# Performance work log

Hardware: AMD Instinct MI355X
Metric: run time of the kernel (lower is better)

Reference implementation:

```python
import jax, jax.numpy as jnp
import numpy as np

DIM = 1024
HEADS = 16
DIM_HEAD = 64
INNER = HEADS * DIM_HEAD  # 1024
EPS = 1e-5


def setup_inputs() -> dict:
    key = jax.random.key(0)
    ks = jax.random.split(key, 5)
    x = jax.random.normal(ks[0], (4, 2048, DIM), dtype=jnp.float32)
    ln_gamma = jnp.ones((DIM,), dtype=jnp.float32)
    ln_beta = jnp.zeros((DIM,), dtype=jnp.float32)
    # nn.Linear weights ~ U(-1/sqrt(fan_in), 1/sqrt(fan_in)); stored as (out, in) in torch,
    # here kept as (in, out) for x @ W.
    lim = 1.0 / np.sqrt(DIM)
    w_qkv = jax.random.uniform(ks[1], (DIM, 3 * INNER), minval=-lim, maxval=lim, dtype=jnp.float32)
    lim2 = 1.0 / np.sqrt(INNER)
    w_out = jax.random.uniform(ks[2], (INNER, DIM), minval=-lim2, maxval=lim2, dtype=jnp.float32)
    return {"x": x, "ln_gamma": ln_gamma, "ln_beta": ln_beta, "w_qkv": w_qkv, "w_out": w_out}


def reference(x, ln_gamma, ln_beta, w_qkv, w_out):
    b, n, d = x.shape
    # LayerNorm
    mu = jnp.mean(x, axis=-1, keepdims=True)
    var = jnp.mean(jnp.square(x - mu), axis=-1, keepdims=True)
    xn = (x - mu) * jax.lax.rsqrt(var + EPS) * ln_gamma + ln_beta
    # QKV projection
    qkv = xn @ w_qkv  # (b, n, 3*inner)
    q, k, v = jnp.split(qkv, 3, axis=-1)
    def to_heads(t):
        return t.reshape(b, n, HEADS, DIM_HEAD).transpose(0, 2, 1, 3)  # (b,h,n,dh)
    q, k, v = to_heads(q), to_heads(k), to_heads(v)
    scale = DIM_HEAD ** -0.5
    scores = jnp.einsum('bhqd,bhkd->bhqk', q, k) * scale
    causal = jnp.tril(jnp.ones((n, n), dtype=bool))
    scores = jnp.where(causal, scores, -jnp.inf)
    probs = jax.nn.softmax(scores, axis=-1)
    out = jnp.einsum('bhqk,bhkd->bhqd', probs, v)
    out = out.transpose(0, 2, 1, 3).reshape(b, n, INNER)
    return out @ w_out
```

## Files before the change

### kernel.cpp

```cpp
#include <hip/hip_runtime.h>
#include <hip/hip_bf16.h>

#define DIM 1024
#define HEADS 16
#define DH 64
#define SEQ 2048
#define BATCH 4
#define ROWS (BATCH * SEQ)
#define NQKV (3 * DIM)

typedef __attribute__((ext_vector_type(8))) __bf16 bf16x8;
typedef __attribute__((ext_vector_type(4))) __bf16 bf16x4;
typedef __attribute__((ext_vector_type(4))) float f32x4;

__device__ inline void gload16(const void* g, void* l) {
  __builtin_amdgcn_global_load_lds(
      (const __attribute__((address_space(1))) void*)g,
      (__attribute__((address_space(3))) void*)l, 16, 0, 0);
}

__device__ inline float fast_exp2(float x) {
#if __has_builtin(__builtin_amdgcn_exp2f)
  return __builtin_amdgcn_exp2f(x);
#else
  return exp2f(x);
#endif
}

__global__ __launch_bounds__(256) void ln_kernel(
    const float* __restrict__ x, const float* __restrict__ gamma,
    const float* __restrict__ beta, __bf16* __restrict__ xnb) {
  const int row = blockIdx.x;
  const int tid = threadIdx.x;
  const float4* xr = (const float4*)(x + (size_t)row * DIM);
  float4 v = xr[tid];
  float s1 = v.x + v.y + v.z + v.w;
  float s2 = v.x * v.x + v.y * v.y + v.z * v.z + v.w * v.w;
#pragma unroll
  for (int d = 32; d > 0; d >>= 1) {
    s1 += __shfl_xor(s1, d);
    s2 += __shfl_xor(s2, d);
  }
  __shared__ float red1[4], red2[4];
  const int wave = tid >> 6, lane = tid & 63;
  if (lane == 0) { red1[wave] = s1; red2[wave] = s2; }
  __syncthreads();
  s1 = red1[0] + red1[1] + red1[2] + red1[3];
  s2 = red2[0] + red2[1] + red2[2] + red2[3];
  const float mean = s1 * (1.0f / DIM);
  const float var = s2 * (1.0f / DIM) - mean * mean;
  const float rstd = rsqrtf(var + 1e-5f);
  float4 g = ((const float4*)gamma)[tid];
  float4 b = ((const float4*)beta)[tid];
  bf16x4 o;
  o[0] = (__bf16)((v.x - mean) * rstd * g.x + b.x);
  o[1] = (__bf16)((v.y - mean) * rstd * g.y + b.y);
  o[2] = (__bf16)((v.z - mean) * rstd * g.z + b.z);
  o[3] = (__bf16)((v.w - mean) * rstd * g.w + b.w);
  *(bf16x4*)(xnb + (size_t)row * DIM + tid * 4) = o;
}

__global__ __launch_bounds__(256) void transpose_cast(
    const float* __restrict__ in, __bf16* __restrict__ outT, int rows, int cols) {
  __shared__ float tile[32][33];
  const int tx = threadIdx.x & 31, ty = threadIdx.x >> 5;
  const int c0 = blockIdx.x * 32, r0 = blockIdx.y * 32;
#pragma unroll
  for (int rr = ty; rr < 32; rr += 8)
    tile[rr][tx] = in[(size_t)(r0 + rr) * cols + c0 + tx];
  __syncthreads();
#pragma unroll
  for (int rr = ty; rr < 32; rr += 8)
    outT[(size_t)(c0 + rr) * rows + r0 + tx] = (__bf16)tile[tx][rr];
}

template <int MODE>
__global__ __launch_bounds__(512, 1) void gemmP(
    const __bf16* __restrict__ A, const __bf16* __restrict__ Bt, const int K,
    const int N, float* __restrict__ Cout, __bf16* __restrict__ qb,
    __bf16* __restrict__ kb, __bf16* __restrict__ vtb) {
  __shared__ __bf16 As[2][2][128 * 64];
  __shared__ __bf16 Bs[2][128 * 64];
  const int tid = threadIdx.x;
  const int wave = tid >> 6, lane = tid & 63;
  const int quad = lane >> 4, l16 = lane & 15;
  const int wm = wave >> 2, wn = wave & 3;

  const int nwg = (int)gridDim.x;
  const int cpx = nwg >> 3;
  const int wg = ((int)blockIdx.x & 7) * cpx + ((int)blockIdx.x >> 3);
  const size_t tileM = (size_t)(wg & 31) * 256;
  const size_t tileN = (size_t)(wg >> 5) * 128;
  const int sel = (MODE == 1) ? (int)(tileN >> 10) : 0;
  const bool vmode = (MODE == 1) && (sel == 2);

  f32x4 acc[8][2];
#pragma unroll
  for (int i = 0; i < 8; ++i)
#pragma unroll
    for (int j = 0; j < 2; ++j) acc[i][j] = (f32x4){0.f, 0.f, 0.f, 0.f};

  const __bf16* Abase = A + tileM * (size_t)K;
  const __bf16* Bbase = Bt + tileN * (size_t)K;

  const int slr = tid >> 3, sc = tid & 7;
  const int scol = (sc ^ (slr & 7)) << 3;

  auto stageA = [&](int buf, int h, int kt) {
    const size_t col = (size_t)(kt << 6) + scol;
#pragma unroll
    for (int p = 0; p < 2; ++p) {
      const int gr = p * 128 + h * 64 + slr;
      const int lr = p * 64 + slr;
      gload16(Abase + (size_t)gr * K + col, &As[buf][h][lr * 64 + sc * 8]);
    }
  };
  auto stageB = [&](int buf, int kt) {
    const size_t col = (size_t)(kt << 6) + scol;
#pragma unroll
    for (int p = 0; p < 2; ++p) {
      const int lr = p * 64 + slr;
      gload16(Bbase + (size_t)lr * K + col, &Bs[buf][lr * 64 + sc * 8]);
    }
  };

  const int rpc = quad ^ (l16 & 7);
  auto ldA = [&](int buf, int mt, int ks) -> bf16x8 {
    const int lr = wm * 64 + (mt & 3) * 16 + l16;
    return *(const bf16x8*)&As[buf][mt >> 2][lr * 64 + ((rpc ^ (ks << 2)) << 3)];
  };
  auto ldB = [&](int buf, int nt, int ks) -> bf16x8 {
    const int lr = wn * 32 + nt * 16 + l16;
    return *(const bf16x8*)&Bs[buf][lr * 64 + ((rpc ^ (ks << 2)) << 3)];
  };

  auto cluster = [&](const bf16x8* af, bf16x8 bf0, bf16x8 bf1, int mb) {
    __builtin_amdgcn_s_setprio(1);
    if (vmode) {
#pragma unroll
      for (int mt = 0; mt < 4; ++mt) {
        acc[mb + mt][0] = __builtin_amdgcn_mfma_f32_16x16x32_bf16(
            af[mt], bf0, acc[mb + mt][0], 0, 0, 0);
        acc[mb + mt][1] = __builtin_amdgcn_mfma_f32_16x16x32_bf16(
            af[mt], bf1, acc[mb + mt][1], 0, 0, 0);
      }
    } else {
#pragma unroll
      for (int mt = 0; mt < 4; ++mt) {
        acc[mb + mt][0] = __builtin_amdgcn_mfma_f32_16x16x32_bf16(
            bf0, af[mt], acc[mb + mt][0], 0, 0, 0);
        acc[mb + mt][1] = __builtin_amdgcn_mfma_f32_16x16x32_bf16(
            bf1, af[mt], acc[mb + mt][1], 0, 0, 0);
      }
    }
    __builtin_amdgcn_s_setprio(0);
  };

  stageA(0, 0, 0);
  stageB(0, 0);
  stageA(0, 1, 0);

  const int NT = K >> 6;
  bf16x8 af[4], b00, b01, b10, b11;

  for (int t = 0; t < NT - 1; ++t) {
    const int buf = t & 1, nbuf = buf ^ 1, kn = t + 1;
    stageA(nbuf, 0, kn);
    asm volatile("s_waitcnt vmcnt(4)" ::: "memory");
    __builtin_amdgcn_s_barrier();
    asm volatile("" ::: "memory");
    __builtin_amdgcn_sched_barrier(0);
#pragma unroll
    for (int mt = 0; mt < 4; ++mt) af[mt] = ldA(buf, mt, 0);
    b00 = ldB(buf, 0, 0);
    b01 = ldB(buf, 1, 0);
    cluster(af, b00, b01, 0);
    stageB(nbuf, kn);
#pragma unroll
    for (int mt = 0; mt < 4; ++mt) af[mt] = ldA(buf, mt, 1);
    b10 = ldB(buf, 0, 1);
    b11 = ldB(buf, 1, 1);
    cluster(af, b10, b11, 0);
    stageA(nbuf, 1, kn);
    asm volatile("s_waitcnt vmcnt(6)" ::: "memory");
    __builtin_amdgcn_s_barrier();
    asm volatile("" ::: "memory");
    __builtin_amdgcn_sched_barrier(0);
#pragma unroll
    for (int mt = 0; mt < 4; ++mt) af[mt] = ldA(buf, 4 + mt, 0);
    cluster(af, b00, b01, 4);
#pragma unroll
    for (int mt = 0; mt < 4; ++mt) af[mt] = ldA(buf, 4 + mt, 1);
    cluster(af, b10, b11, 4);
  }

  {
    const int buf = (NT - 1) & 1;
    asm volatile("s_waitcnt vmcnt(2)" ::: "memory");
    __builtin_amdgcn_s_barrier();
    asm volatile("" ::: "memory");
    __builtin_amdgcn_sched_barrier(0);
#pragma unroll
    for (int mt = 0; mt < 4; ++mt) af[mt] = ldA(buf, mt, 0);
    b00 = ldB(buf, 0, 0);
    b01 = ldB(buf, 1, 0);
    cluster(af, b00, b01, 0);
#pragma unroll
    for (int mt = 0; mt < 4; ++mt) af[mt] = ldA(buf, mt, 1);
    b10 = ldB(buf, 0, 1);
    b11 = ldB(buf, 1, 1);
    cluster(af, b10, b11, 0);
    asm volatile("s_waitcnt vmcnt(0)" ::: "memory");
    __builtin_amdgcn_s_barrier();
    asm volatile("" ::: "memory");
    __builtin_amdgcn_sched_barrier(0);
#pragma unroll
    for (int mt = 0; mt < 4; ++mt) af[mt] = ldA(buf, 4 + mt, 0);
    cluster(af, b00, b01, 4);
#pragma unroll
    for (int mt = 0; mt < 4; ++mt) af[mt] = ldA(buf, 4 + mt, 1);
    cluster(af, b10, b11, 4);
  }

  if (MODE == 0) {
#pragma unroll
    for (int mt = 0; mt < 8; ++mt) {
      const size_t m = tileM + wm * 128 + mt * 16 + l16;
#pragma unroll
      for (int nt = 0; nt < 2; ++nt) {
        const size_t n0 = tileN + wn * 32 + nt * 16 + quad * 4;
        *(f32x4*)&Cout[m * (size_t)N + n0] = acc[mt][nt];
      }
    }
  } else if (sel < 2) {
    __bf16* dst = (sel == 0) ? qb : kb;
#pragma unroll
    for (int mt = 0; mt < 8; ++mt) {
      const size_t m = tileM + wm * 128 + mt * 16 + l16;
      const int b = (int)(m >> 11), seq = (int)(m & 2047);
#pragma unroll
      for (int nt = 0; nt < 2; ++nt) {
        const int c = (int)(tileN & 1023) + wn * 32 + nt * 16 + quad * 4;
        const int head = c >> 6, dh = c & 63;
        bf16x4 pk;
#pragma unroll
        for (int r = 0; r < 4; ++r) pk[r] = (__bf16)acc[mt][nt][r];
        *(bf16x4*)&dst[(((size_t)b * HEADS + head) * SEQ + seq) * DH + dh] = pk;
      }
    }
  } else {
#pragma unroll
    for (int nt = 0; nt < 2; ++nt) {
      const int c = (int)(tileN & 1023) + wn * 32 + nt * 16 + l16;
      const int head = c >> 6, dh = c & 63;
#pragma unroll
      for (int mt = 0; mt < 8; ++mt) {
        const size_t m0 = tileM + wm * 128 + mt * 16 + quad * 4;
        const int b = (int)(m0 >> 11), seq = (int)(m0 & 2047);
        bf16x4 pk;
#pragma unroll
        for (int r = 0; r < 4; ++r) pk[r] = (__bf16)acc[mt][nt][r];
        *(bf16x4*)&vtb[(((size_t)b * HEADS + head) * DH + dh) * SEQ + seq] = pk;
      }
    }
  }
}

__global__ __launch_bounds__(256, 4) void attn_kernel(
    const __bf16* __restrict__ qb, const __bf16* __restrict__ kb,
    const __bf16* __restrict__ vtb, __bf16* __restrict__ ob) {
  const int bh = blockIdx.x;
  const int by = blockIdx.y;
  const int tid = threadIdx.x;
  const int wave = tid >> 6, lane = tid & 63;
  const int quad = lane >> 4, l16 = lane & 15;

  __shared__ __bf16 Ks[2][64 * 64];
  __shared__ __bf16 Vs[2][64 * 64];
  __shared__ __bf16 Ps[4][16 * 36];

  const __bf16* kg = kb + (size_t)bh * SEQ * DH;
  const __bf16* vg = vtb + (size_t)bh * DH * SEQ;

  const int i1 = by, i2 = 31 - by;
  const int T = 33;

  const int kr = lane >> 3, kc = lane & 7;

  auto stage = [&](int buf, int j) {
#pragma unroll
    for (int p = 0; p < 2; ++p) {
      const int rbase = wave * 16 + p * 8;
      const int row = rbase + kr;
      gload16(kg + (size_t)(j * 64 + row) * DH + ((kc ^ (row & 7)) << 3),
              &Ks[buf][rbase * 64]);
      gload16(vg + (size_t)row * SEQ + j * 64 + ((kc ^ (row & 7)) << 3),
              &Vs[buf][rbase * 64]);
    }
  };

  const float QSCALE = 0.125f * 1.44269504088896f;
  bf16x8 qf[2];
  auto load_q = [&](int i) {
    const __bf16* qbase = qb + ((size_t)bh * SEQ + (size_t)i * 64 + wave * 16) * DH;
#pragma unroll
    for (int ks = 0; ks < 2; ++ks) {
      bf16x8 v = *(const bf16x8*)(qbase + l16 * DH + ks * 32 + quad * 8);
#pragma unroll
      for (int e = 0; e < 8; ++e) v[e] = (__bf16)((float)v[e] * QSCALE);
      qf[ks] = v;
    }
  };

  float m_i, l_i;
  f32x4 o_acc[4];
  auto reset_state = [&]() {
    m_i = -1e30f;
    l_i = 0.f;
#pragma unroll
    for (int md = 0; md < 4; ++md) o_acc[md] = (f32x4){0.f, 0.f, 0.f, 0.f};
  };
  const int b_out = bh >> 4, h_out = bh & 15;
  auto epilogue = [&](int i) {
    float lsum = l_i;
    lsum += __shfl_xor(lsum, 16);
    lsum += __shfl_xor(lsum, 32);
    const float inv = __builtin_amdgcn_rcpf(lsum);
    const int seq = i * 64 + wave * 16 + l16;
    __bf16* dst = ob + ((size_t)b_out * SEQ + seq) * DIM + h_out * DH;
#pragma unroll
    for (int md = 0; md < 4; ++md) {
      bf16x4 pk;
#pragma unroll
      for (int r = 0; r < 4; ++r) pk[r] = (__bf16)(o_acc[md][r] * inv);
      *(bf16x4*)(dst + md * 16 + quad * 4) = pk;
    }
  };

  load_q(i1);
  reset_state();
  stage(0, 0);

  for (int t = 0; t < T; ++t) {
    __syncthreads();
    if (t + 1 < T) {
      const int jn = (t + 1 <= by) ? (t + 1) : (t - by);
      stage((t + 1) & 1, jn);
    }
    const int buf = t & 1;
    const int i = (t <= by) ? i1 : i2;
    const int j = (t <= by) ? t : (t - by - 1);
    const bool diag = (j == i);

    f32x4 sa[4];
#pragma unroll
    for (int nt = 0; nt < 4; ++nt) sa[nt] = (f32x4){0.f, 0.f, 0.f, 0.f};
#pragma unroll
    for (int nt = 0; nt < 4; ++nt)
#pragma unroll
      for (int ks = 0; ks < 2; ++ks) {
        bf16x8 kf = *(const bf16x8*)&Ks[buf][(nt * 16 + l16) * 64 +
                                            (((ks * 4 + quad) ^ (l16 & 7)) << 3)];
        sa[nt] = __builtin_amdgcn_mfma_f32_16x16x32_bf16(kf, qf[ks], sa[nt], 0, 0, 0);
      }

    if (diag) {
      const int qrl = wave * 16 + l16;
#pragma unroll
      for (int nt = 0; nt < 4; ++nt)
#pragma unroll
        for (int r = 0; r < 4; ++r) {
          const int kvl = nt * 16 + quad * 4 + r;
          if (kvl > qrl) sa[nt][r] = -1e30f;
        }
    }

    {
      float mx = -1e30f;
#pragma unroll
      for (int nt = 0; nt < 4; ++nt) {
        const float a0 = fmaxf(fmaxf(sa[nt][0], sa[nt][1]), sa[nt][2]);
        mx = fmaxf(mx, fmaxf(a0, sa[nt][3]));
      }
      mx = fmaxf(mx, __shfl_xor(mx, 16));
      mx = fmaxf(mx, __shfl_xor(mx, 32));
      if (__all(mx - m_i <= 8.f)) {
        float rs = 0.f;
#pragma unroll
        for (int nt = 0; nt < 4; ++nt)
#pragma unroll
          for (int r = 0; r < 4; ++r) {
            const float p = fast_exp2(sa[nt][r] - m_i);
            sa[nt][r] = p;
            rs += p;
          }
        l_i += rs;
      } else {
        const float mnew = fmaxf(m_i, mx);
        const float alpha = fast_exp2(m_i - mnew);
        m_i = mnew;
        float rs = 0.f;
#pragma unroll
        for (int nt = 0; nt < 4; ++nt)
#pragma unroll
          for (int r = 0; r < 4; ++r) {
            const float p = fast_exp2(sa[nt][r] - mnew);
            sa[nt][r] = p;
            rs += p;
          }
        l_i = l_i * alpha + rs;
#pragma unroll
        for (int md = 0; md < 4; ++md)
#pragma unroll
          for (int r = 0; r < 4; ++r) o_acc[md][r] *= alpha;
      }
    }

#pragma unroll
    for (int c = 0; c < 2; ++c) {
#pragma unroll
      for (int ntl = 0; ntl < 2; ++ntl) {
        const int nt = c * 2 + ntl;
        bf16x4 pk;
#pragma unroll
        for (int r = 0; r < 4; ++r) pk[r] = (__bf16)sa[nt][r];
        *(bf16x4*)&Ps[wave][l16 * 36 + ntl * 16 + quad * 4] = pk;
      }
      bf16x8 pf = *(const bf16x8*)&Ps[wave][l16 * 36 + quad * 8];
#pragma unroll
      for (int md = 0; md < 4; ++md) {
        bf16x8 vf = *(const bf16x8*)&Vs[buf][(md * 16 + l16) * 64 +
                                            (((c * 4 + quad) ^ (l16 & 7)) << 3)];
        o_acc[md] = __builtin_amdgcn_mfma_f32_16x16x32_bf16(vf, pf, o_acc[md], 0, 0, 0);
      }
    }

    if (t == by) {
      epilogue(i1);
      reset_state();
      load_q(i2);
    }
  }
  epilogue(i2);
}

extern "C" void kernel_launch(void* const* d_in, const int* in_sizes, int n_in,
                              void* d_out, int out_size, void* d_ws, size_t ws_size,
                              hipStream_t stream) {
  const float* x = (const float*)d_in[0];
  const float* gamma = (const float*)d_in[1];
  const float* beta = (const float*)d_in[2];
  const float* w_qkv = (const float*)d_in[3];
  const float* w_out = (const float*)d_in[4];
  float* out = (float*)d_out;

  char* ws = (char*)d_ws;
  const size_t MB = 1024 * 1024;
  __bf16* xnb = (__bf16*)ws;
  __bf16* wqkvT = (__bf16*)(ws + 16 * MB);
  __bf16* woutT = (__bf16*)(ws + 24 * MB);
  __bf16* qbuf = (__bf16*)(ws + 32 * MB);
  __bf16* kbuf = (__bf16*)(ws + 48 * MB);
  __bf16* vtbuf = (__bf16*)(ws + 64 * MB);
  __bf16* attnb = xnb;

  ln_kernel<<<ROWS, 256, 0, stream>>>(x, gamma, beta, xnb);
  transpose_cast<<<dim3(NQKV / 32, DIM / 32), 256, 0, stream>>>(w_qkv, wqkvT, DIM, NQKV);
  transpose_cast<<<dim3(DIM / 32, DIM / 32), 256, 0, stream>>>(w_out, woutT, DIM, DIM);
  gemmP<1><<<dim3((ROWS / 256) * (NQKV / 128)), 512, 0, stream>>>(
      xnb, wqkvT, DIM, NQKV, nullptr, qbuf, kbuf, vtbuf);
  attn_kernel<<<dim3(BATCH * HEADS, 16), 256, 0, stream>>>(qbuf, kbuf, vtbuf, attnb);
  gemmP<0><<<dim3((ROWS / 256) * (DIM / 128)), 512, 0, stream>>>(
      attnb, woutT, DIM, DIM, out, nullptr, nullptr, nullptr);
}
```

Before: 285.5 us.

## Triple-buffer GEMM K-loop, drop XCD swizzle, fuse weight transposes

The GEMM mainloop moves from a double-buffered, split-phase pipeline to a three-stage ring buffer that prefetches two K tiles ahead, with one barrier per iteration instead of two. The goal is to hide global-to-LDS latency better and cut synchronisation. LDS use grows to 144 KB per workgroup. The XCD-aware workgroup remapping is replaced by a plain 2D grid, which may hurt L2 locality across XCDs. The two weight transpose-cast launches are merged into one kernel to save a launch.

```diff
diff --git a/kernel.cpp b/kernel.cpp
--- a/kernel.cpp
+++ b/kernel.cpp
@@ -60,18 +60,28 @@
   *(bf16x4*)(xnb + (size_t)row * DIM + tid * 4) = o;
 }
 
-__global__ __launch_bounds__(256) void transpose_cast(
-    const float* __restrict__ in, __bf16* __restrict__ outT, int rows, int cols) {
+__global__ __launch_bounds__(256) void transpose_cast2(
+    const float* __restrict__ wq, const float* __restrict__ wo,
+    __bf16* __restrict__ qT, __bf16* __restrict__ oT) {
   __shared__ float tile[32][33];
   const int tx = threadIdx.x & 31, ty = threadIdx.x >> 5;
-  const int c0 = blockIdx.x * 32, r0 = blockIdx.y * 32;
+  int bx = blockIdx.x;
+  const float* in;
+  __bf16* out;
+  int cols;
+  if (bx < 96) {
+    in = wq; out = qT; cols = NQKV;
+  } else {
+    in = wo; out = oT; cols = DIM; bx -= 96;
+  }
+  const int c0 = bx * 32, r0 = blockIdx.y * 32;
 #pragma unroll
   for (int rr = ty; rr < 32; rr += 8)
     tile[rr][tx] = in[(size_t)(r0 + rr) * cols + c0 + tx];
   __syncthreads();
 #pragma unroll
   for (int rr = ty; rr < 32; rr += 8)
-    outT[(size_t)(c0 + rr) * rows + r0 + tx] = (__bf16)tile[tx][rr];
+    out[(size_t)(c0 + rr) * DIM + r0 + tx] = (__bf16)tile[tx][rr];
 }
 
 template <int MODE>
@@ -79,18 +89,15 @@
     const __bf16* __restrict__ A, const __bf16* __restrict__ Bt, const int K,
     const int N, float* __restrict__ Cout, __bf16* __restrict__ qb,
     __bf16* __restrict__ kb, __bf16* __restrict__ vtb) {
-  __shared__ __bf16 As[2][2][128 * 64];
-  __shared__ __bf16 Bs[2][128 * 64];
+  __shared__ __bf16 As[3][2][128 * 64];
+  __shared__ __bf16 Bs[3][128 * 64];
   const int tid = threadIdx.x;
   const int wave = tid >> 6, lane = tid & 63;
   const int quad = lane >> 4, l16 = lane & 15;
   const int wm = wave >> 2, wn = wave & 3;
 
-  const int nwg = (int)gridDim.x;
-  const int cpx = nwg >> 3;
-  const int wg = ((int)blockIdx.x & 7) * cpx + ((int)blockIdx.x >> 3);
-  const size_t tileM = (size_t)(wg & 31) * 256;
-  const size_t tileN = (size_t)(wg >> 5) * 128;
+  const size_t tileM = (size_t)blockIdx.x * 256;
+  const size_t tileN = (size_t)blockIdx.y * 128;
   const int sel = (MODE == 1) ? (int)(tileN >> 10) : 0;
   const bool vmode = (MODE == 1) && (sel == 2);
 
@@ -122,6 +129,11 @@
       const int lr = p * 64 + slr;
       gload16(Bbase + (size_t)lr * K + col, &Bs[buf][lr * 64 + sc * 8]);
     }
+  };
+  auto stageTile = [&](int buf, int kt) {
+    stageA(buf, 0, kt);
+    stageB(buf, kt);
+    stageA(buf, 1, kt);
   };
 
   const int rpc = quad ^ (l16 & 7);
@@ -156,70 +168,45 @@
     __builtin_amdgcn_s_setprio(0);
   };
 
-  stageA(0, 0, 0);
-  stageB(0, 0);
-  stageA(0, 1, 0);
+  stageTile(0, 0);
+  stageTile(1, 1);
 
   const int NT = K >> 6;
+  int bufc = 0;
   bf16x8 af[4], b00, b01, b10, b11;
 
-  for (int t = 0; t < NT - 1; ++t) {
-    const int buf = t & 1, nbuf = buf ^ 1, kn = t + 1;
-    stageA(nbuf, 0, kn);
-    asm volatile("s_waitcnt vmcnt(4)" ::: "memory");
+  for (int t = 0; t < NT; ++t) {
+    if (t < NT - 1)
+      asm volatile("s_waitcnt vmcnt(6)" ::: "memory");
+    else
+      asm volatile("s_waitcnt vmcnt(0)" ::: "memory");
     __builtin_amdgcn_s_barrier();
     asm volatile("" ::: "memory");
     __builtin_amdgcn_sched_barrier(0);
-#pragma unroll
-    for (int mt = 0; mt < 4; ++mt) af[mt] = ldA(buf, mt, 0);
-    b00 = ldB(buf, 0, 0);
-    b01 = ldB(buf, 1, 0);
+
+    if (t + 2 < NT) {
+      const int sb = bufc + 2 >= 3 ? bufc - 1 : bufc + 2;
+      stageTile(sb, t + 2);
+    }
+
+#pragma unroll
+    for (int mt = 0; mt < 4; ++mt) af[mt] = ldA(bufc, mt, 0);
+    b00 = ldB(bufc, 0, 0);
+    b01 = ldB(bufc, 1, 0);
     cluster(af, b00, b01, 0);
-    stageB(nbuf, kn);
-#pragma unroll
-    for (int mt = 0; mt < 4; ++mt) af[mt] = ldA(buf, mt, 1);
-    b10 = ldB(buf, 0, 1);
-    b11 = ldB(buf, 1, 1);
+#pragma unroll
+    for (int mt = 0; mt < 4; ++mt) af[mt] = ldA(bufc, mt, 1);
+    b10 = ldB(bufc, 0, 1);
+    b11 = ldB(bufc, 1, 1);
     cluster(af, b10, b11, 0);
-    stageA(nbuf, 1, kn);
-    asm volatile("s_waitcnt vmcnt(6)" ::: "memory");
-    __builtin_amdgcn_s_barrier();
-    asm volatile("" ::: "memory");
-    __builtin_amdgcn_sched_barrier(0);
-#pragma unroll
-    for (int mt = 0; mt < 4; ++mt) af[mt] = ldA(buf, 4 + mt, 0);
+#pragma unroll
+    for (int mt = 0; mt < 4; ++mt) af[mt] = ldA(bufc, 4 + mt, 0);
     cluster(af, b00, b01, 4);
 #pragma unroll
-    for (int mt = 0; mt < 4; ++mt) af[mt] = ldA(buf, 4 + mt, 1);
+    for (int mt = 0; mt < 4; ++mt) af[mt] = ldA(bufc, 4 + mt, 1);
     cluster(af, b10, b11, 4);
-  }
-
-  {
-    const int buf = (NT - 1) & 1;
-    asm volatile("s_waitcnt vmcnt(2)" ::: "memory");
-    __builtin_amdgcn_s_barrier();
-    asm volatile("" ::: "memory");
-    __builtin_amdgcn_sched_barrier(0);
-#pragma unroll
-    for (int mt = 0; mt < 4; ++mt) af[mt] = ldA(buf, mt, 0);
-    b00 = ldB(buf, 0, 0);
-    b01 = ldB(buf, 1, 0);
-    cluster(af, b00, b01, 0);
-#pragma unroll
-    for (int mt = 0; mt < 4; ++mt) af[mt] = ldA(buf, mt, 1);
-    b10 = ldB(buf, 0, 1);
-    b11 = ldB(buf, 1, 1);
-    cluster(af, b10, b11, 0);
-    asm volatile("s_waitcnt vmcnt(0)" ::: "memory");
-    __builtin_amdgcn_s_barrier();
-    asm volatile("" ::: "memory");
-    __builtin_amdgcn_sched_barrier(0);
-#pragma unroll
-    for (int mt = 0; mt < 4; ++mt) af[mt] = ldA(buf, 4 + mt, 0);
-    cluster(af, b00, b01, 4);
-#pragma unroll
-    for (int mt = 0; mt < 4; ++mt) af[mt] = ldA(buf, 4 + mt, 1);
-    cluster(af, b10, b11, 4);
+
+    bufc = bufc == 2 ? 0 : bufc + 1;
   }
 
   if (MODE == 0) {
@@ -465,11 +452,10 @@
   __bf16* attnb = xnb;
 
   ln_kernel<<<ROWS, 256, 0, stream>>>(x, gamma, beta, xnb);
-  transpose_cast<<<dim3(NQKV / 32, DIM / 32), 256, 0, stream>>>(w_qkv, wqkvT, DIM, NQKV);
-  transpose_cast<<<dim3(DIM / 32, DIM / 32), 256, 0, stream>>>(w_out, woutT, DIM, DIM);
-  gemmP<1><<<dim3((ROWS / 256) * (NQKV / 128)), 512, 0, stream>>>(
+  transpose_cast2<<<dim3(128, 32), 256, 0, stream>>>(w_qkv, w_out, wqkvT, woutT);
+  gemmP<1><<<dim3(ROWS / 256, NQKV / 128), 512, 0, stream>>>(
       xnb, wqkvT, DIM, NQKV, nullptr, qbuf, kbuf, vtbuf);
   attn_kernel<<<dim3(BATCH * HEADS, 16), 256, 0, stream>>>(qbuf, kbuf, vtbuf, attnb);
-  gemmP<0><<<dim3((ROWS / 256) * (DIM / 128)), 512, 0, stream>>>(
+  gemmP<0><<<dim3(ROWS / 256, DIM / 128), 512, 0, stream>>>(
       attnb, woutT, DIM, DIM, out, nullptr, nullptr, nullptr);
 }
```

New measurement: 271.7 us. 1.05x faster.
